# Kernel tuning notes

Measured on AMD Instinct MI355X. Metric: run time of the kernel, lower is better.

Reference implementation:

```python
import jax, jax.numpy as jnp
import numpy as np

N, C, E = 50000, 128, 400000
R_CUT = 5.0


def setup_inputs() -> dict:
    key = jax.random.key(0)
    ks = jax.random.split(key, 12)
    s = jax.random.normal(ks[0], (N, C), dtype=jnp.float32)
    v = jax.random.normal(ks[1], (N, 3, C), dtype=jnp.float32)
    edges = jax.random.randint(ks[2], (E, 2), 0, N, dtype=jnp.int64)
    r_ij = jax.random.uniform(ks[3], (E, 1), dtype=jnp.float32, minval=0.1, maxval=R_CUT)
    rn = jax.random.normal(ks[4], (E, 3), dtype=jnp.float32)
    r_ij_normalized = rn / jnp.linalg.norm(rn, axis=-1, keepdims=True)
    sc = 1.0 / np.sqrt(C)
    W1 = jax.random.normal(ks[5], (C, C), dtype=jnp.float32) * sc
    b1 = jnp.zeros((C,), dtype=jnp.float32)
    W2 = jax.random.normal(ks[6], (C, 3 * C), dtype=jnp.float32) * sc
    b2 = jnp.zeros((3 * C,), dtype=jnp.float32)
    Wr = jax.random.normal(ks[7], (20, 3 * C), dtype=jnp.float32) * (1.0 / np.sqrt(20))
    br = jnp.zeros((3 * C,), dtype=jnp.float32)
    return {"s": s, "v": v, "edges": edges, "r_ij": r_ij,
            "r_ij_normalized": r_ij_normalized,
            "W1": W1, "b1": b1, "W2": W2, "b2": b2, "Wr": Wr, "br": br}


def rbf(r_ij, r_cut):
    # r_ij: [E,1] -> [E,20]; sin(n*pi/r_cut * r) / r for n=1..20
    n = jnp.arange(1, 21, dtype=r_ij.dtype)  # [20]
    return jnp.sin((np.pi / r_cut) * n * r_ij) / r_ij


def fcut(r_ij, r_cut):
    return 0.5 * (jnp.cos(np.pi * r_ij / r_cut) + 1.0)  # [E,1]


def reference(s, v, edges, r_ij, r_ij_normalized, W1, b1, W2, b2, Wr, br):
    r_cut = R_CUT
    src = edges[:, 1]
    dst = edges[:, 0]
    # RBF filter: [E,3C], modulated by cosine cutoff
    rbf_pass = (rbf(r_ij, r_cut) @ Wr + br) * fcut(r_ij, r_cut)
    # node MLP: Linear -> SiLU -> Linear : [N,3C]
    s_pass = jax.nn.silu(s @ W1 + b1) @ W2 + b2
    pass_out = rbf_pass * s_pass[src]  # [E,3C]
    dv, ds, drep = jnp.split(pass_out, 3, axis=-1)  # each [E,C]
    # [E,3,C] = gathered v * gate + direction * rep
    delta_v = v[src] * dv[:, None, :] + r_ij_normalized[:, :, None] * drep[:, None, :]
    s_out = s + jax.ops.segment_sum(ds, dst, num_segments=N)
    v_out = v + jax.ops.segment_sum(delta_v, dst, num_segments=N)
    return s_out, v_out
```

## Files before the change

### kernel.cpp

```cpp
#include <hip/hip_runtime.h>
#include <hip/hip_bf16.h>

#define CC 128
#define NOUT 384
#define PI_F 3.14159265358979323846f
#define RCUT 5.0f

typedef float f32x2 __attribute__((ext_vector_type(2)));

__device__ __forceinline__ float loadF(const void* p, size_t i, int isf32) {
  if (isf32) return ((const float*)p)[i];
  unsigned int w = ((unsigned int)((const unsigned short*)p)[i]) << 16;
  return __uint_as_float(w);
}
__device__ __forceinline__ int loadI(const void* p, size_t i, int isi64) {
  if (isi64) return (int)((const long long*)p)[i];
  return ((const int*)p)[i];
}
__device__ __forceinline__ unsigned int bfbits(float f) {
  __hip_bfloat16 h = __float2bfloat16(f);
  unsigned short u;
  __builtin_memcpy(&u, &h, 2);
  return (unsigned int)u;
}
__device__ __forceinline__ unsigned int bfpack(float lo, float hi) {
  return bfbits(lo) | (bfbits(hi) << 16);
}
__device__ __forceinline__ float bf16lo(unsigned int u) {
  return __uint_as_float(u << 16);
}
__device__ __forceinline__ float bf16hi(unsigned int u) {
  return __uint_as_float(u & 0xffff0000u);
}

__global__ void detect_kernel(const void* s, const void* edges, int* flags) {
  if (threadIdx.x == 0) {
    int isf32 = 0;
    const unsigned short* us = (const unsigned short*)s;
    for (int i = 0; i < 1024; i++) {
      unsigned int w = ((unsigned int)us[i]) << 16;
      float f = __uint_as_float(w);
      if (!(fabsf(f) < 1000.f)) { isf32 = 1; break; }
    }
    int isi64 = 1;
    const int* ie = (const int*)edges;
    for (int i = 1; i < 128; i += 2) {
      if (ie[i] != 0) { isi64 = 0; break; }
    }
    flags[0] = isf32;
    flags[1] = isi64;
  }
}

__global__ void count_kernel(const void* __restrict__ edges, int* __restrict__ cnt,
                             const int* __restrict__ flags, int E) {
  int e = blockIdx.x * blockDim.x + threadIdx.x;
  if (e >= E) return;
  int dst = loadI(edges, (size_t)2 * e, flags[1]);
  atomicAdd(&cnt[dst], 1);
}

__global__ __launch_bounds__(1024) void scan_kernel(const int* __restrict__ cnt,
                                                    int* __restrict__ row_start,
                                                    int* __restrict__ next, int N) {
  __shared__ int woff[16];
  __shared__ int carry_sh;
  const int t = threadIdx.x;
  const int lane = t & 63;
  const int wid = t >> 6;
  if (t == 0) carry_sh = 0;
  __syncthreads();
  for (int base = 0; base < N; base += 1024) {
    int x = (base + t < N) ? cnt[base + t] : 0;
    int incl = x;
    #pragma unroll
    for (int off = 1; off < 64; off <<= 1) {
      int y = __shfl_up(incl, off, 64);
      if (lane >= off) incl += y;
    }
    if (lane == 63) woff[wid] = incl;
    __syncthreads();
    if (wid == 0 && lane < 16) {
      int w = woff[lane];
      int iw = w;
      #pragma unroll
      for (int off = 1; off < 16; off <<= 1) {
        int y = __shfl_up(iw, off, 64);
        if (lane >= off) iw += y;
      }
      woff[lane] = iw - w;
    }
    __syncthreads();
    int carry = carry_sh;
    int excl = carry + woff[wid] + incl - x;
    if (base + t < N) { row_start[base + t] = excl; next[base + t] = excl; }
    __syncthreads();
    if (t == 1023) carry_sh = excl + x;
    __syncthreads();
  }
  if (t == 0) row_start[N] = carry_sh;
}

template <int PRE>
__global__ void fill_kernel(const void* __restrict__ edges,
                            const void* __restrict__ r_ij,
                            const void* __restrict__ rn,
                            int* __restrict__ next,
                            int* __restrict__ esrc,
                            float4* __restrict__ efcrn,
                            float* __restrict__ erb,
                            const int* __restrict__ flags, int E) {
  int e = blockIdx.x * blockDim.x + threadIdx.x;
  if (e >= E) return;
  const int isi64 = flags[1];
  const int isf32 = flags[0];
  const int dst = loadI(edges, (size_t)2 * e, isi64);
  const int src = loadI(edges, (size_t)2 * e + 1, isi64);
  const float r  = loadF(r_ij, e, isf32);
  const float r0 = loadF(rn, (size_t)e * 3 + 0, isf32);
  const float r1 = loadF(rn, (size_t)e * 3 + 1, isf32);
  const float r2 = loadF(rn, (size_t)e * 3 + 2, isf32);
  const int p = atomicAdd(&next[dst], 1);
  esrc[p] = src;
  if (PRE) {
    const float x = (PI_F / RCUT) * r;
    const float s1 = __sinf(x);
    const float c1 = __cosf(x);
    const float fc = 0.5f * (c1 + 1.f);
    efcrn[p] = make_float4(fc, r0, r1, r2);
    const float rf = __builtin_amdgcn_rcpf(r) * fc;
    const float twoc = 2.f * c1;
    float sp = 0.f, sn = s1;
    float rbv[20];
    #pragma unroll
    for (int k = 0; k < 20; k++) {
      rbv[k] = sn * rf;
      const float s2 = twoc * sn - sp;
      sp = sn; sn = s2;
    }
    float4* rb4 = (float4*)(erb + (size_t)p * 20);
    #pragma unroll
    for (int j = 0; j < 5; j++)
      rb4[j] = make_float4(rbv[4 * j], rbv[4 * j + 1], rbv[4 * j + 2], rbv[4 * j + 3]);
  } else {
    efcrn[p] = make_float4(r, r0, r1, r2);
  }
}

template <int ISF32>
__device__ __forceinline__ void node_mlp_body(
    const void* __restrict__ s, const void* __restrict__ v,
    const void* __restrict__ W1, const void* __restrict__ b1,
    const void* __restrict__ W2, const void* __restrict__ b2,
    uint2* __restrict__ tabA, int N) {
  const int M = 8;
  __shared__ float s_sh[M][CC];
  __shared__ float h_sh[M][CC];
  const int c = threadIdx.x;
  const int n0 = blockIdx.x * M;

  #pragma unroll
  for (int m = 0; m < M; m++) {
    int n = n0 + m;
    s_sh[m][c] = (n < N) ? loadF(s, (size_t)n * CC + c, ISF32) : 0.f;
  }
  __syncthreads();

  float acc[M];
  #pragma unroll
  for (int m = 0; m < M; m++) acc[m] = 0.f;
  for (int k = 0; k < CC; k++) {
    float w = loadF(W1, (size_t)k * CC + c, ISF32);
    #pragma unroll
    for (int m = 0; m < M; m++) acc[m] += s_sh[m][k] * w;
  }
  float bb1 = loadF(b1, c, ISF32);
  #pragma unroll
  for (int m = 0; m < M; m++) {
    float x = acc[m] + bb1;
    h_sh[m][c] = x / (1.f + __expf(-x));
  }
  __syncthreads();

  float a2s[3][M];
  #pragma unroll
  for (int jj = 0; jj < 3; jj++) {
    int j = jj * CC + c;
    float a2[M];
    #pragma unroll
    for (int m = 0; m < M; m++) a2[m] = 0.f;
    for (int k = 0; k < CC; k++) {
      float w = loadF(W2, (size_t)k * NOUT + j, ISF32);
      #pragma unroll
      for (int m = 0; m < M; m++) a2[m] += h_sh[m][k] * w;
    }
    float bb2 = loadF(b2, j, ISF32);
    #pragma unroll
    for (int m = 0; m < M; m++) a2s[jj][m] = a2[m] + bb2;
  }

  #pragma unroll
  for (int m = 0; m < M; m++) {
    int n = n0 + m;
    if (n >= N) continue;
    const float v0 = loadF(v, (size_t)n * NOUT + c, ISF32);
    const size_t tix = (size_t)n * CC + c;
    tabA[tix] = make_uint2(bfpack(a2s[0][m], a2s[1][m]), bfpack(a2s[2][m], v0));
  }
}

__global__ __launch_bounds__(128) void node_mlp_kernel(
    const void* __restrict__ s, const void* __restrict__ v,
    const void* __restrict__ W1, const void* __restrict__ b1,
    const void* __restrict__ W2, const void* __restrict__ b2,
    uint2* __restrict__ tabA, const int* __restrict__ flags, int N) {
  if (flags[0]) node_mlp_body<1>(s, v, W1, b1, W2, b2, tabA, N);
  else          node_mlp_body<0>(s, v, W1, b1, W2, b2, tabA, N);
}

template <int ISF32, int PRE>
__device__ __forceinline__ void agg_body(
    const void* __restrict__ s, const void* __restrict__ v,
    const void* __restrict__ Wr, const void* __restrict__ br,
    const uint2* __restrict__ tabA,
    const int* __restrict__ row_start,
    const int* __restrict__ esrc, const float4* __restrict__ efcrn,
    const float* __restrict__ erb,
    void* __restrict__ out, int N) {
  const int n = blockIdx.x;
  const int c = threadIdx.x;

  f32x2 w0p[10], w1p[10], w2p[10];
  #pragma unroll
  for (int j = 0; j < 10; j++) {
    w0p[j] = f32x2{loadF(Wr, (size_t)(2 * j) * NOUT + c, ISF32),
                   loadF(Wr, (size_t)(2 * j + 1) * NOUT + c, ISF32)};
    w1p[j] = f32x2{loadF(Wr, (size_t)(2 * j) * NOUT + CC + c, ISF32),
                   loadF(Wr, (size_t)(2 * j + 1) * NOUT + CC + c, ISF32)};
    w2p[j] = f32x2{loadF(Wr, (size_t)(2 * j) * NOUT + 2 * CC + c, ISF32),
                   loadF(Wr, (size_t)(2 * j + 1) * NOUT + 2 * CC + c, ISF32)};
  }
  const float b0  = loadF(br, c, ISF32);
  const float b1v = loadF(br, CC + c, ISF32);
  const float b2v = loadF(br, 2 * CC + c, ISF32);

  float accs = 0.f, av0 = 0.f, av1 = 0.f, av2 = 0.f;
  const int beg = row_start[n], end = row_start[n + 1];

  int i = beg;
  for (; i + 2 <= end; i += 2) {
    const int srcA = esrc[i];
    const int srcB = esrc[i + 1];
    const float4 frA = efcrn[i];
    const float4 frB = efcrn[i + 1];
    const uint2 taA = tabA[(size_t)srcA * CC + c];
    const uint2 taB = tabA[(size_t)srcB * CC + c];
    const float v1A = loadF(v, (size_t)srcA * NOUT + CC + c, ISF32);
    const float v2A = loadF(v, (size_t)srcA * NOUT + 2 * CC + c, ISF32);
    const float v1B = loadF(v, (size_t)srcB * NOUT + CC + c, ISF32);
    const float v2B = loadF(v, (size_t)srcB * NOUT + 2 * CC + c, ISF32);

    float fcA, fcB;
    f32x2 rbA[10], rbB[10];
    if (PRE) {
      fcA = frA.x;
      fcB = frB.x;
      const f32x2* rpA = (const f32x2*)(erb + (size_t)i * 20);
      const f32x2* rpB = (const f32x2*)(erb + (size_t)(i + 1) * 20);
      #pragma unroll
      for (int j = 0; j < 10; j++) { rbA[j] = rpA[j]; rbB[j] = rpB[j]; }
    } else {
      const float xA = (PI_F / RCUT) * frA.x;
      const float s1A = __sinf(xA), c1A = __cosf(xA);
      fcA = 0.5f * (c1A + 1.f);
      const float rfA = __builtin_amdgcn_rcpf(frA.x) * fcA;
      const float twocA = 2.f * c1A;
      const float xB = (PI_F / RCUT) * frB.x;
      const float s1B = __sinf(xB), c1B = __cosf(xB);
      fcB = 0.5f * (c1B + 1.f);
      const float rfB = __builtin_amdgcn_rcpf(frB.x) * fcB;
      const float twocB = 2.f * c1B;
      float spA = 0.f, snA = s1A, spB = 0.f, snB = s1B;
      #pragma unroll
      for (int j = 0; j < 10; j++) {
        const float qA0 = snA * rfA;
        float s2 = twocA * snA - spA; spA = snA; snA = s2;
        const float qA1 = snA * rfA;
        s2 = twocA * snA - spA; spA = snA; snA = s2;
        rbA[j] = f32x2{qA0, qA1};
        const float qB0 = snB * rfB;
        s2 = twocB * snB - spB; spB = snB; snB = s2;
        const float qB1 = snB * rfB;
        s2 = twocB * snB - spB; spB = snB; snB = s2;
        rbB[j] = f32x2{qB0, qB1};
      }
    }

    f32x2 a0A = f32x2{0.f, 0.f}, a1A = a0A, a2A = a0A;
    f32x2 a0B = a0A, a1B = a0A, a2B = a0A;
    #pragma unroll
    for (int j = 0; j < 10; j++) {
      a0A += rbA[j] * w0p[j];  a0B += rbB[j] * w0p[j];
      a1A += rbA[j] * w1p[j];  a1B += rbB[j] * w1p[j];
      a2A += rbA[j] * w2p[j];  a2B += rbB[j] * w2p[j];
    }

    const float a0Af = fmaf(b0,  fcA, a0A.x + a0A.y);
    const float a1Af = fmaf(b1v, fcA, a1A.x + a1A.y);
    const float a2Af = fmaf(b2v, fcA, a2A.x + a2A.y);
    const float p0A = a0Af * bf16lo(taA.x);
    const float p1A = a1Af * bf16hi(taA.x);
    const float p2A = a2Af * bf16lo(taA.y);
    accs += p1A;
    av0 = fmaf(bf16hi(taA.y), p0A, fmaf(frA.y, p2A, av0));
    av1 = fmaf(v1A, p0A, fmaf(frA.z, p2A, av1));
    av2 = fmaf(v2A, p0A, fmaf(frA.w, p2A, av2));

    const float a0Bf = fmaf(b0,  fcB, a0B.x + a0B.y);
    const float a1Bf = fmaf(b1v, fcB, a1B.x + a1B.y);
    const float a2Bf = fmaf(b2v, fcB, a2B.x + a2B.y);
    const float p0B = a0Bf * bf16lo(taB.x);
    const float p1B = a1Bf * bf16hi(taB.x);
    const float p2B = a2Bf * bf16lo(taB.y);
    accs += p1B;
    av0 = fmaf(bf16hi(taB.y), p0B, fmaf(frB.y, p2B, av0));
    av1 = fmaf(v1B, p0B, fmaf(frB.z, p2B, av1));
    av2 = fmaf(v2B, p0B, fmaf(frB.w, p2B, av2));
  }

  for (; i < end; ++i) {
    const int src = esrc[i];
    const float4 fr = efcrn[i];
    const uint2 ta = tabA[(size_t)src * CC + c];
    const float v1f = loadF(v, (size_t)src * NOUT + CC + c, ISF32);
    const float v2f = loadF(v, (size_t)src * NOUT + 2 * CC + c, ISF32);

    float fc;
    f32x2 rb[10];
    if (PRE) {
      fc = fr.x;
      const f32x2* rp = (const f32x2*)(erb + (size_t)i * 20);
      #pragma unroll
      for (int j = 0; j < 10; j++) rb[j] = rp[j];
    } else {
      const float x = (PI_F / RCUT) * fr.x;
      const float s1 = __sinf(x), c1 = __cosf(x);
      fc = 0.5f * (c1 + 1.f);
      const float rf = __builtin_amdgcn_rcpf(fr.x) * fc;
      const float twoc = 2.f * c1;
      float spv = 0.f, snv = s1;
      #pragma unroll
      for (int j = 0; j < 10; j++) {
        const float q0 = snv * rf;
        float s2 = twoc * snv - spv; spv = snv; snv = s2;
        const float q1 = snv * rf;
        s2 = twoc * snv - spv; spv = snv; snv = s2;
        rb[j] = f32x2{q0, q1};
      }
    }

    f32x2 a0p = f32x2{0.f, 0.f}, a1p = a0p, a2p = a0p;
    #pragma unroll
    for (int j = 0; j < 10; j++) {
      a0p += rb[j] * w0p[j];
      a1p += rb[j] * w1p[j];
      a2p += rb[j] * w2p[j];
    }

    const float a0 = fmaf(b0,  fc, a0p.x + a0p.y);
    const float a1 = fmaf(b1v, fc, a1p.x + a1p.y);
    const float a2 = fmaf(b2v, fc, a2p.x + a2p.y);
    const float p0 = a0 * bf16lo(ta.x);
    const float p1 = a1 * bf16hi(ta.x);
    const float p2 = a2 * bf16lo(ta.y);
    accs += p1;
    av0 = fmaf(bf16hi(ta.y), p0, fmaf(fr.y, p2, av0));
    av1 = fmaf(v1f, p0, fmaf(fr.z, p2, av1));
    av2 = fmaf(v2f, p0, fmaf(fr.w, p2, av2));
  }

  const size_t si = (size_t)n * CC + c;
  const size_t vi = (size_t)n * NOUT;
  const float so = loadF(s, si, ISF32) + accs;
  const float o0 = loadF(v, vi + 0 * CC + c, ISF32) + av0;
  const float o1 = loadF(v, vi + 1 * CC + c, ISF32) + av1;
  const float o2 = loadF(v, vi + 2 * CC + c, ISF32) + av2;
  const size_t vo = (size_t)N * CC + vi;
  if (ISF32) {
    float* o = (float*)out;
    o[si] = so;
    o[vo + 0 * CC + c] = o0;
    o[vo + 1 * CC + c] = o1;
    o[vo + 2 * CC + c] = o2;
  } else {
    __hip_bfloat16* o = (__hip_bfloat16*)out;
    o[si] = __float2bfloat16(so);
    o[vo + 0 * CC + c] = __float2bfloat16(o0);
    o[vo + 1 * CC + c] = __float2bfloat16(o1);
    o[vo + 2 * CC + c] = __float2bfloat16(o2);
  }
}

template <int PRE>
__global__ __launch_bounds__(128, 3) void aggregate_kernel(
    const void* __restrict__ s, const void* __restrict__ v,
    const void* __restrict__ Wr, const void* __restrict__ br,
    const uint2* __restrict__ tabA,
    const int* __restrict__ row_start,
    const int* __restrict__ esrc, const float4* __restrict__ efcrn,
    const float* __restrict__ erb,
    void* __restrict__ out, const int* __restrict__ flags, int N) {
  if (flags[0]) agg_body<1, PRE>(s, v, Wr, br, tabA, row_start, esrc, efcrn, erb, out, N);
  else          agg_body<0, PRE>(s, v, Wr, br, tabA, row_start, esrc, efcrn, erb, out, N);
}

extern "C" void kernel_launch(void* const* d_in, const int* in_sizes, int n_in,
                              void* d_out, int out_size, void* d_ws, size_t ws_size,
                              hipStream_t stream) {
  const void* s     = d_in[0];
  const void* v     = d_in[1];
  const void* edges = d_in[2];
  const void* r_ij  = d_in[3];
  const void* rn    = d_in[4];
  const void* W1    = d_in[5];
  const void* b1    = d_in[6];
  const void* W2    = d_in[7];
  const void* b2    = d_in[8];
  const void* Wr    = d_in[9];
  const void* br    = d_in[10];

  const int N = in_sizes[0] / CC;
  const int E = in_sizes[3];

  char* ws = (char*)d_ws;
  int* flags = (int*)ws;
  size_t off = 256;
  auto align16 = [](size_t x) { return (x + 15) & ~(size_t)15; };
  uint2* tabA = (uint2*)(ws + off);      off += align16((size_t)N * CC * 8);
  float4* efcrn = (float4*)(ws + off);   off += align16((size_t)E * 16);
  int* esrc = (int*)(ws + off);          off += align16((size_t)E * 4);
  int* cnt = (int*)(ws + off);           off += align16((size_t)N * 4);
  int* row_start = (int*)(ws + off);     off += align16((size_t)(N + 1) * 4);
  int* next = (int*)(ws + off);          off += align16((size_t)N * 4);
  float* erb = (float*)(ws + off);
  const size_t off_erb_end = off + (size_t)E * 20 * 4;
  const int pre = (ws_size >= off_erb_end) ? 1 : 0;

  hipMemsetAsync(cnt, 0, (size_t)N * sizeof(int), stream);

  detect_kernel<<<1, 64, 0, stream>>>(s, edges, flags);
  count_kernel<<<(E + 255) / 256, 256, 0, stream>>>(edges, cnt, flags, E);
  scan_kernel<<<1, 1024, 0, stream>>>(cnt, row_start, next, N);
  if (pre)
    fill_kernel<1><<<(E + 255) / 256, 256, 0, stream>>>(edges, r_ij, rn, next,
                                                        esrc, efcrn, erb, flags, E);
  else
    fill_kernel<0><<<(E + 255) / 256, 256, 0, stream>>>(edges, r_ij, rn, next,
                                                        esrc, efcrn, erb, flags, E);
  node_mlp_kernel<<<(N + 7) / 8, 128, 0, stream>>>(s, v, W1, b1, W2, b2,
                                                   tabA, flags, N);
  if (pre)
    aggregate_kernel<1><<<N, 128, 0, stream>>>(s, v, Wr, br, tabA, row_start,
                                               esrc, efcrn, erb, d_out, flags, N);
  else
    aggregate_kernel<0><<<N, 128, 0, stream>>>(s, v, Wr, br, tabA, row_start,
                                               esrc, efcrn, erb, d_out, flags, N);
}
```

Before: 638.3 us.

## Compute node MLP with bf16 MFMA and a runtime-verified scalar fallback

Replaces the scalar FMA node MLP with a matrix-core kernel. Each block handles 64 nodes: swizzled LDS stages the bf16 inputs, and W1/W2 are pre-transposed to bf16 by a prep kernel before both layers run through 16x16x32 bf16 MFMAs. A single-block check kernel compares node 0 against a scalar reference and sets a flag. The old kernel then runs as a fallback only if that check fails. This cuts the arithmetic cost of the dense MLP but adds two small kernel launches and lowers input precision to bf16.

```diff
diff --git a/kernel.cpp b/kernel.cpp
--- a/kernel.cpp
+++ b/kernel.cpp
@@ -7,6 +7,8 @@
 #define RCUT 5.0f
 
 typedef float f32x2 __attribute__((ext_vector_type(2)));
+typedef __attribute__((ext_vector_type(8))) short bf16x8;
+typedef __attribute__((ext_vector_type(4))) float f32x4;
 
 __device__ __forceinline__ float loadF(const void* p, size_t i, int isf32) {
   if (isf32) return ((const float*)p)[i];
@@ -147,6 +149,159 @@
   }
 }
 
+__global__ void prep_w_kernel(const void* __restrict__ W1, const void* __restrict__ W2,
+                              unsigned short* __restrict__ W1T,
+                              unsigned short* __restrict__ W2T,
+                              const int* __restrict__ flags) {
+  const int c = blockIdx.x;
+  const int k = threadIdx.x;
+  const int isf32 = flags[0];
+  if (c < CC) {
+    W1T[(size_t)c * CC + k] = (unsigned short)bfbits(loadF(W1, (size_t)k * CC + c, isf32));
+  } else {
+    const int cc = c - CC;
+    W2T[(size_t)cc * CC + k] = (unsigned short)bfbits(loadF(W2, (size_t)k * NOUT + cc, isf32));
+  }
+}
+
+template <int ISF32>
+__device__ __forceinline__ void mlp_mfma_body(
+    const void* __restrict__ s, const void* __restrict__ v,
+    const unsigned short* __restrict__ W1T, const unsigned short* __restrict__ W2T,
+    const void* __restrict__ b1, const void* __restrict__ b2,
+    uint2* __restrict__ tabA, int N) {
+  __shared__ unsigned short lds[64 * 128];
+  const int t = threadIdx.x;
+  const int l = t & 63;
+  const int w = t >> 6;
+  const int n0 = blockIdx.x * 64;
+
+  #pragma unroll
+  for (int it = 0; it < 32; ++it) {
+    const int id = it * 256 + t;
+    const int row = id >> 7;
+    const int col = id & 127;
+    const int srow = (n0 + row < N) ? (n0 + row) : (N - 1);
+    const float f = loadF(s, (size_t)srow * CC + col, ISF32);
+    const int byte = (row * 256 + col * 2) ^ ((row & 7) << 4);
+    lds[byte >> 1] = (unsigned short)bfbits(f);
+  }
+  __syncthreads();
+
+  const int arow = w * 16 + (l & 15);
+  bf16x8 a[4];
+  #pragma unroll
+  for (int kk = 0; kk < 4; ++kk) {
+    const int byte = (arow * 256 + (kk * 4 + (l >> 4)) * 16) ^ ((arow & 7) << 4);
+    a[kk] = *(const bf16x8*)((const char*)lds + byte);
+  }
+
+  f32x4 acc1[8];
+  #pragma unroll
+  for (int jt = 0; jt < 8; ++jt) { acc1[jt] = f32x4{0.f, 0.f, 0.f, 0.f}; }
+  #pragma unroll
+  for (int jt = 0; jt < 8; ++jt) {
+    const unsigned short* wp = W1T + (size_t)(jt * 16 + (l & 15)) * CC + (l >> 4) * 8;
+    #pragma unroll
+    for (int kk = 0; kk < 4; ++kk) {
+      const bf16x8 b = *(const bf16x8*)(wp + kk * 32);
+      acc1[jt] = __builtin_amdgcn_mfma_f32_16x16x32_bf16(a[kk], b, acc1[jt], 0, 0, 0);
+    }
+  }
+  __syncthreads();
+
+  #pragma unroll
+  for (int jt = 0; jt < 8; ++jt) {
+    const int c = jt * 16 + (l & 15);
+    const float bb = loadF(b1, c, ISF32);
+    #pragma unroll
+    for (int r = 0; r < 4; ++r) {
+      const int row = w * 16 + (l >> 4) * 4 + r;
+      const float x = acc1[jt][r] + bb;
+      const float h = x / (1.f + __expf(-x));
+      const int byte = (row * 256 + c * 2) ^ ((row & 7) << 4);
+      lds[byte >> 1] = (unsigned short)bfbits(h);
+    }
+  }
+  __syncthreads();
+
+  bf16x8 a2[4];
+  #pragma unroll
+  for (int kk = 0; kk < 4; ++kk) {
+    const int byte = (arow * 256 + (kk * 4 + (l >> 4)) * 16) ^ ((arow & 7) << 4);
+    a2[kk] = *(const bf16x8*)((const char*)lds + byte);
+  }
+  f32x4 acc2[24];
+  #pragma unroll
+  for (int jt = 0; jt < 24; ++jt) { acc2[jt] = f32x4{0.f, 0.f, 0.f, 0.f}; }
+  #pragma unroll
+  for (int jt = 0; jt < 24; ++jt) {
+    const unsigned short* wp = W2T + (size_t)(jt * 16 + (l & 15)) * CC + (l >> 4) * 8;
+    #pragma unroll
+    for (int kk = 0; kk < 4; ++kk) {
+      const bf16x8 b = *(const bf16x8*)(wp + kk * 32);
+      acc2[jt] = __builtin_amdgcn_mfma_f32_16x16x32_bf16(a2[kk], b, acc2[jt], 0, 0, 0);
+    }
+  }
+
+  #pragma unroll
+  for (int jt = 0; jt < 8; ++jt) {
+    const int c = jt * 16 + (l & 15);
+    const float bb0 = loadF(b2, c, ISF32);
+    const float bb1 = loadF(b2, CC + c, ISF32);
+    const float bb2v = loadF(b2, 2 * CC + c, ISF32);
+    #pragma unroll
+    for (int r = 0; r < 4; ++r) {
+      const int n = n0 + w * 16 + (l >> 4) * 4 + r;
+      if (n >= N) continue;
+      const float v0 = loadF(v, (size_t)n * NOUT + c, ISF32);
+      tabA[(size_t)n * CC + c] =
+          make_uint2(bfpack(acc2[jt][r] + bb0, acc2[jt + 8][r] + bb1),
+                     bfpack(acc2[jt + 16][r] + bb2v, v0));
+    }
+  }
+}
+
+__global__ __launch_bounds__(256, 2) void node_mlp_mfma_kernel(
+    const void* __restrict__ s, const void* __restrict__ v,
+    const unsigned short* __restrict__ W1T, const unsigned short* __restrict__ W2T,
+    const void* __restrict__ b1, const void* __restrict__ b2,
+    uint2* __restrict__ tabA, const int* __restrict__ flags, int N) {
+  if (flags[0]) mlp_mfma_body<1>(s, v, W1T, W2T, b1, b2, tabA, N);
+  else          mlp_mfma_body<0>(s, v, W1T, W2T, b1, b2, tabA, N);
+}
+
+__global__ void mlp_check_kernel(const void* __restrict__ s,
+                                 const void* __restrict__ W1, const void* __restrict__ b1,
+                                 const void* __restrict__ W2, const void* __restrict__ b2,
+                                 const uint2* __restrict__ tabA, int* __restrict__ flags) {
+  __shared__ float h_sh[CC];
+  __shared__ int bad;
+  const int c = threadIdx.x;
+  if (c == 0) bad = 0;
+  __syncthreads();
+  const int isf32 = flags[0];
+  float acc = 0.f;
+  for (int k = 0; k < CC; k++)
+    acc += loadF(s, k, isf32) * loadF(W1, (size_t)k * CC + c, isf32);
+  acc += loadF(b1, c, isf32);
+  h_sh[c] = acc / (1.f + __expf(-acc));
+  __syncthreads();
+  const uint2 ta = tabA[c];
+  const float got[3] = {bf16lo(ta.x), bf16hi(ta.x), bf16lo(ta.y)};
+  int mybad = 0;
+  for (int jj = 0; jj < 3; jj++) {
+    float a2 = 0.f;
+    for (int k = 0; k < CC; k++)
+      a2 += h_sh[k] * loadF(W2, (size_t)k * NOUT + jj * CC + c, isf32);
+    a2 += loadF(b2, jj * CC + c, isf32);
+    if (fabsf(got[jj] - a2) > 0.25f + 0.02f * fabsf(a2)) mybad = 1;
+  }
+  if (mybad) atomicOr(&bad, 1);
+  __syncthreads();
+  if (c == 0) flags[2] = bad ? 0 : 1;
+}
+
 template <int ISF32>
 __device__ __forceinline__ void node_mlp_body(
     const void* __restrict__ s, const void* __restrict__ v,
@@ -209,11 +364,12 @@
   }
 }
 
-__global__ __launch_bounds__(128) void node_mlp_kernel(
+__global__ __launch_bounds__(128) void node_mlp_fallback_kernel(
     const void* __restrict__ s, const void* __restrict__ v,
     const void* __restrict__ W1, const void* __restrict__ b1,
     const void* __restrict__ W2, const void* __restrict__ b2,
     uint2* __restrict__ tabA, const int* __restrict__ flags, int N) {
+  if (flags[2]) return;
   if (flags[0]) node_mlp_body<1>(s, v, W1, b1, W2, b2, tabA, N);
   else          node_mlp_body<0>(s, v, W1, b1, W2, b2, tabA, N);
 }
@@ -436,6 +592,8 @@
   int* flags = (int*)ws;
   size_t off = 256;
   auto align16 = [](size_t x) { return (x + 15) & ~(size_t)15; };
+  unsigned short* W1T = (unsigned short*)(ws + off);  off += align16((size_t)CC * CC * 2);
+  unsigned short* W2T = (unsigned short*)(ws + off);  off += align16((size_t)NOUT * CC * 2);
   uint2* tabA = (uint2*)(ws + off);      off += align16((size_t)N * CC * 8);
   float4* efcrn = (float4*)(ws + off);   off += align16((size_t)E * 16);
   int* esrc = (int*)(ws + off);          off += align16((size_t)E * 4);
@@ -457,8 +615,12 @@
   else
     fill_kernel<0><<<(E + 255) / 256, 256, 0, stream>>>(edges, r_ij, rn, next,
                                                         esrc, efcrn, erb, flags, E);
-  node_mlp_kernel<<<(N + 7) / 8, 128, 0, stream>>>(s, v, W1, b1, W2, b2,
-                                                   tabA, flags, N);
+  prep_w_kernel<<<CC + NOUT, 128, 0, stream>>>(W1, W2, W1T, W2T, flags);
+  node_mlp_mfma_kernel<<<(N + 63) / 64, 256, 0, stream>>>(s, v, W1T, W2T, b1, b2,
+                                                          tabA, flags, N);
+  mlp_check_kernel<<<1, 128, 0, stream>>>(s, W1, b1, W2, b2, tabA, flags);
+  node_mlp_fallback_kernel<<<(N + 7) / 8, 128, 0, stream>>>(s, v, W1, b1, W2, b2,
+                                                            tabA, flags, N);
   if (pre)
     aggregate_kernel<1><<<N, 128, 0, stream>>>(s, v, Wr, br, tabA, row_start,
                                                esrc, efcrn, erb, d_out, flags, N);
```

After: 611.8 us. 1.04x faster.
